# Kernel optimization log

Measured on AMD Instinct MI355X. Metric: run time of the kernel, lower is better.

Reference implementation:

```python
import math
import jax, jax.numpy as jnp
import numpy as np

N_NODES = 100000
N_EDGES = 1600000
IN_DIM, HID_DIM, OUT_DIM = 8, 64, 112


def _glorot(key, fan_in, fan_out):
    lim = math.sqrt(6.0 / (fan_in + fan_out))
    return jax.random.uniform(key, (fan_in, fan_out), jnp.float32, -lim, lim)


def _layer_params(key, in_d, out_d):
    ks = jax.random.split(key, 8)
    return dict(
        Wq=_glorot(ks[0], in_d, out_d), bq=jnp.zeros((out_d,), jnp.float32),
        Wk=_glorot(ks[1], in_d, out_d), bk=jnp.zeros((out_d,), jnp.float32),
        Wv=_glorot(ks[2], in_d, out_d), bv=jnp.zeros((out_d,), jnp.float32),
        Ws=_glorot(ks[3], in_d, out_d), bs=jnp.zeros((out_d,), jnp.float32),
    )


def setup_inputs() -> dict:
    key = jax.random.key(0)
    kx, ke, k0, k1, k2 = jax.random.split(key, 5)
    inp = {
        'x': jax.random.normal(kx, (N_NODES, IN_DIM), jnp.float32),
        'edge_index': jax.random.randint(ke, (2, N_EDGES), 0, N_NODES, jnp.int64),
    }
    for li, (kk, ind, outd) in enumerate([(k0, IN_DIM, HID_DIM), (k1, HID_DIM, HID_DIM), (k2, HID_DIM, OUT_DIM)]):
        p = _layer_params(kk, ind, outd)
        for name, v in p.items():
            inp[f'{name}{li}'] = v
    return inp


def _transformer_conv(x, src, dst, Wq, bq, Wk, bk, Wv, bv, Ws, bs):
    # heads=1, concat=True, no edge_attr, eval mode (no dropout)
    N = x.shape[0]
    C = Wq.shape[1]
    q = x @ Wq + bq            # [N, C]
    k = x @ Wk + bk
    v = x @ Wv + bv
    # per-edge attention score: <q_dst, k_src> / sqrt(C)
    scores = jnp.sum(q[dst] * k[src], axis=-1) * (1.0 / math.sqrt(C))  # [E]
    # segment softmax over destination neighborhoods (stable)
    m = jax.ops.segment_max(scores, dst, num_segments=N)               # [N]
    e = jnp.exp(scores - m[dst])                                       # [E]
    denom = jax.ops.segment_sum(e, dst, num_segments=N)                # [N]
    alpha = e / denom[dst]                                             # [E]
    # weighted scatter-add of source values to destinations
    out = jax.ops.segment_sum(alpha[:, None] * v[src], dst, num_segments=N)  # [N, C]
    # root/skip connection
    return out + (x @ Ws + bs)


def reference(x, edge_index,
              Wq0, bq0, Wk0, bk0, Wv0, bv0, Ws0, bs0,
              Wq1, bq1, Wk1, bk1, Wv1, bv1, Ws1, bs1,
              Wq2, bq2, Wk2, bk2, Wv2, bv2, Ws2, bs2):
    src, dst = edge_index[0], edge_index[1]
    h = _transformer_conv(x, src, dst, Wq0, bq0, Wk0, bk0, Wv0, bv0, Ws0, bs0)
    h = jax.nn.relu(h)
    h = _transformer_conv(h, src, dst, Wq1, bq1, Wk1, bk1, Wv1, bv1, Ws1, bs1)
    h = jax.nn.relu(h)
    out = _transformer_conv(h, src, dst, Wq2, bq2, Wk2, bk2, Wv2, bv2, Ws2, bs2)
    return out
```

## Files before the change

kernel.cpp:

```cpp
#include <hip/hip_runtime.h>
#include <hip/hip_fp16.h>
#include <math.h>
#include <float.h>
#include <stdint.h>

#define NN 100000
#define NE 1600000

#define SCAN_T 256
#define SCAN_E 1024
#define SCAN_NB ((NN + SCAN_E - 1) / SCAN_E)

#define NBUCK ((NN + 255) / 256)
#define EPB   4096
#define NBLK  ((NE + EPB - 1) / EPB)
#define HISTN (NBUCK * NBLK)
#define GS_NB ((HISTN + SCAN_E - 1) / SCAN_E)
#define BCAP  5120

typedef __attribute__((ext_vector_type(8))) short short8v;
typedef __attribute__((ext_vector_type(4))) float float4v;

__device__ __forceinline__ unsigned short f32_to_bf16_rne(float f) {
    unsigned u = __float_as_uint(f);
    u += 0x7FFFu + ((u >> 16) & 1u);
    return (unsigned short)(u >> 16);
}
__device__ __forceinline__ float bf16_to_f32(unsigned short h) {
    return __uint_as_float(((unsigned)h) << 16);
}

template<int K, int OUT>
__global__ __launch_bounds__(256)
void prep_w(const float* __restrict__ Wq, const float* __restrict__ Wk,
            const float* __restrict__ Wv, const float* __restrict__ Ws,
            unsigned short* __restrict__ wsp) {
    constexpr int NKS  = (K + 31) / 32;
    constexpr int OUTT = 4 * OUT;
    constexpr int NCT  = OUTT / 16;
    int idx = blockIdx.x * 256 + threadIdx.x;
    if (idx >= NCT * NKS * 512) return;
    int j    = idx & 7;
    int lane = (idx >> 3) & 63;
    int cell = idx >> 9;
    int ks   = cell % NKS;
    int ct   = cell / NKS;
    int g = lane >> 4, ln = lane & 15;
    int k = ks * 32 + g * 8 + j;
    int c = ct * 16 + ln;
    int mat = c / OUT, cm = c % OUT;
    const float* W = (mat == 0) ? Wq : (mat == 1) ? Wk : (mat == 2) ? Wv : Ws;
    float f = (k < K) ? W[(size_t)k * OUT + cm] : 0.f;
    unsigned short h = f32_to_bf16_rne(f);
    float resid = f - bf16_to_f32(h);
    wsp[(size_t)cell * 1024 + lane * 8 + j]       = h;
    wsp[(size_t)cell * 1024 + 512 + lane * 8 + j] = f32_to_bf16_rne(resid);
}

template<int K, int OUT, int CTSPLIT>
__global__ __launch_bounds__(256)
void gemm_qkvs(const float* __restrict__ x,
               const unsigned short* __restrict__ wsp,
               const float* __restrict__ bq, const float* __restrict__ bk,
               const float* __restrict__ bv, const float* __restrict__ bs,
               float* __restrict__ q, unsigned short* __restrict__ kv,
               float* __restrict__ outskip) {
    constexpr int NKS  = (K + 31) / 32;
    constexpr int OUTT = 4 * OUT;
    constexpr int NCT  = OUTT / 16;
    constexpr int CTPB = NCT / CTSPLIT;

    const int t    = threadIdx.x;
    const int lane = t & 63;
    const int wv   = t >> 6;
    const int g    = lane >> 4;
    const int ln   = lane & 15;
    const int rowbase = (blockIdx.x * 4 + wv) * 32;
    if (rowbase >= NN) return;

    union F8 { short8v v; unsigned short s[8]; uint4 u4; };

    F8 ahi[2][NKS], alo[2][NKS];
#pragma unroll
    for (int rt = 0; rt < 2; ++rt) {
        int r = rowbase + rt * 16 + ln;
        if (r >= NN) r = NN - 1;
        const float* rowp = x + (size_t)r * K;
#pragma unroll
        for (int ks = 0; ks < NKS; ++ks) {
            const int k0 = ks * 32 + g * 8;
            float xv[8];
            if (k0 + 8 <= K) {
                float4 p0 = *(const float4*)(rowp + k0);
                float4 p1 = *(const float4*)(rowp + k0 + 4);
                xv[0] = p0.x; xv[1] = p0.y; xv[2] = p0.z; xv[3] = p0.w;
                xv[4] = p1.x; xv[5] = p1.y; xv[6] = p1.z; xv[7] = p1.w;
            } else {
#pragma unroll
                for (int j = 0; j < 8; ++j) xv[j] = 0.f;
            }
#pragma unroll
            for (int j = 0; j < 8; ++j) {
                unsigned short h = f32_to_bf16_rne(xv[j]);
                ahi[rt][ks].s[j] = h;
                alo[rt][ks].s[j] = f32_to_bf16_rne(xv[j] - bf16_to_f32(h));
            }
        }
    }

    const int ct0 = blockIdx.y * CTPB;
#pragma unroll 1
    for (int ct = ct0; ct < ct0 + CTPB; ++ct) {
        F8 bhi[NKS], blo[NKS];
        const unsigned short* wp = wsp + (size_t)(ct * NKS) * 1024 + lane * 8;
#pragma unroll
        for (int ks = 0; ks < NKS; ++ks) {
            bhi[ks].u4 = *(const uint4*)(wp + ks * 1024);
            blo[ks].u4 = *(const uint4*)(wp + ks * 1024 + 512);
        }

        const int cb  = ct * 16;
        const int mat = cb / OUT;
        const int cm  = (cb % OUT) + ln;
        const float* B = (mat == 0) ? bq : (mat == 1) ? bk : (mat == 2) ? bv : bs;
        const float bias = B[cm];
        float4v acc0 = {bias, bias, bias, bias};
        float4v acc1 = {bias, bias, bias, bias};
#pragma unroll
        for (int ks = 0; ks < NKS; ++ks) {
            acc0 = __builtin_amdgcn_mfma_f32_16x16x32_bf16(ahi[0][ks].v, blo[ks].v, acc0, 0, 0, 0);
            acc0 = __builtin_amdgcn_mfma_f32_16x16x32_bf16(alo[0][ks].v, bhi[ks].v, acc0, 0, 0, 0);
            acc0 = __builtin_amdgcn_mfma_f32_16x16x32_bf16(ahi[0][ks].v, bhi[ks].v, acc0, 0, 0, 0);
            acc1 = __builtin_amdgcn_mfma_f32_16x16x32_bf16(ahi[1][ks].v, blo[ks].v, acc1, 0, 0, 0);
            acc1 = __builtin_amdgcn_mfma_f32_16x16x32_bf16(alo[1][ks].v, bhi[ks].v, acc1, 0, 0, 0);
            acc1 = __builtin_amdgcn_mfma_f32_16x16x32_bf16(ahi[1][ks].v, bhi[ks].v, acc1, 0, 0, 0);
        }

        if (mat == 0 || mat == 3) {
            float* dst = (mat == 0) ? q : outskip;
#pragma unroll
            for (int rt = 0; rt < 2; ++rt) {
                float4v a = rt ? acc1 : acc0;
#pragma unroll
                for (int reg = 0; reg < 4; ++reg) {
                    int node = rowbase + rt * 16 + g * 4 + reg;
                    if (node < NN)
                        dst[(size_t)node * OUT + cm] = a[reg];
                }
            }
        } else {
            const int base = (mat == 1) ? 0 : OUT;
#pragma unroll
            for (int rt = 0; rt < 2; ++rt) {
                float4v a = rt ? acc1 : acc0;
#pragma unroll
                for (int reg = 0; reg < 4; ++reg) {
                    int node = rowbase + rt * 16 + g * 4 + reg;
                    float f = a[reg];
                    float other = __shfl_xor(f, 1);
                    if (node < NN && !(ln & 1)) {
                        unsigned lo16 = __half_as_ushort(__float2half_rn(f));
                        unsigned hi16 = __half_as_ushort(__float2half_rn(other));
                        *(unsigned*)(kv + (size_t)node * (2 * OUT) + base + cm)
                            = lo16 | (hi16 << 16);
                    }
                }
            }
        }
    }
}

__global__ __launch_bounds__(256)
void bin_count(const int* __restrict__ ei, int* __restrict__ hist) {
    __shared__ int h[NBUCK];
    const int t = threadIdx.x;
    for (int i = t; i < NBUCK; i += 256) h[i] = 0;
    __syncthreads();
    int e0 = blockIdx.x * EPB;
    int e1 = e0 + EPB < NE ? e0 + EPB : NE;
    for (int i = e0 + t; i < e1; i += 256)
        atomicAdd(&h[ei[NE + i] >> 8], 1);
    __syncthreads();
    for (int i = t; i < NBUCK; i += 256)
        hist[(size_t)i * NBLK + blockIdx.x] = h[i];
}

__global__ __launch_bounds__(SCAN_T)
void gscan1(int* __restrict__ a, int* __restrict__ bsums) {
    __shared__ int lds[SCAN_T];
    int t = threadIdx.x;
    int base = blockIdx.x * SCAN_E + t * 4;
    int vals[4];
    int s = 0;
#pragma unroll
    for (int j = 0; j < 4; ++j) {
        int idx = base + j;
        vals[j] = (idx < HISTN) ? a[idx] : 0;
        s += vals[j];
    }
    lds[t] = s;
    __syncthreads();
    for (int off = 1; off < SCAN_T; off <<= 1) {
        int xx = (t >= off) ? lds[t - off] : 0;
        __syncthreads();
        lds[t] += xx;
        __syncthreads();
    }
    int run = (t > 0) ? lds[t - 1] : 0;
    if (t == SCAN_T - 1) bsums[blockIdx.x] = lds[t];
#pragma unroll
    for (int j = 0; j < 4; ++j) {
        int idx = base + j;
        if (idx < HISTN) a[idx] = run;
        run += vals[j];
    }
}

__global__ __launch_bounds__(256)
void gscan2(int* __restrict__ bsums) {
    __shared__ int lds[256];
    int t = threadIdx.x;
    lds[t] = (t < GS_NB) ? bsums[t] : 0;
    __syncthreads();
    for (int off = 1; off < 256; off <<= 1) {
        int xx = (t >= off) ? lds[t - off] : 0;
        __syncthreads();
        lds[t] += xx;
        __syncthreads();
    }
    if (t < GS_NB) bsums[t] = (t > 0) ? lds[t - 1] : 0;
}

__global__ __launch_bounds__(256)
void gscan3(int* __restrict__ a, const int* __restrict__ bsums,
            int* __restrict__ bstart) {
    int i = blockIdx.x * 256 + threadIdx.x;
    if (i < HISTN) {
        int v = a[i] + bsums[i / SCAN_E];
        a[i] = v;
        if (i % NBLK == 0) bstart[i / NBLK] = v;
    }
    if (i == 0) bstart[NBUCK] = NE;
}

__global__ __launch_bounds__(256)
void bin_scatter(const int* __restrict__ ei, const int* __restrict__ hist,
                 unsigned* __restrict__ ebuf) {
    __shared__ int off[NBUCK];
    const int t = threadIdx.x;
    for (int i = t; i < NBUCK; i += 256)
        off[i] = hist[(size_t)i * NBLK + blockIdx.x];
    __syncthreads();
    int e0 = blockIdx.x * EPB;
    int e1 = e0 + EPB < NE ? e0 + EPB : NE;
    for (int i = e0 + t; i < e1; i += 256) {
        int src = ei[i];
        int dst = ei[NE + i];
        int b = dst >> 8;
        int p = atomicAdd(&off[b], 1);
        ebuf[p] = ((unsigned)(dst & 255) << 17) | (unsigned)src;
    }
}

__global__ __launch_bounds__(256)
void bucket_hist(const int* __restrict__ bstart,
                 const unsigned* __restrict__ ebuf,
                 int* __restrict__ counts) {
    __shared__ int h[256];
    const int b = blockIdx.x;
    const int t = threadIdx.x;
    h[t] = 0;
    __syncthreads();
    int beg = bstart[b], end = bstart[b + 1];
    for (int i = beg + t; i < end; i += 256)
        atomicAdd(&h[ebuf[i] >> 17], 1);
    __syncthreads();
    int d = b * 256 + t;
    if (d < NN) counts[d] = h[t];
}

__global__ __launch_bounds__(SCAN_T)
void scan1(const int* __restrict__ counts, int* __restrict__ offsets,
           int* __restrict__ blocksums) {
    __shared__ int lds[SCAN_T];
    int t = threadIdx.x;
    int base = blockIdx.x * SCAN_E + t * 4;
    int vals[4];
    int s = 0;
#pragma unroll
    for (int j = 0; j < 4; ++j) {
        int idx = base + j;
        vals[j] = (idx < NN) ? counts[idx] : 0;
        s += vals[j];
    }
    lds[t] = s;
    __syncthreads();
    for (int off = 1; off < SCAN_T; off <<= 1) {
        int xx = (t >= off) ? lds[t - off] : 0;
        __syncthreads();
        lds[t] += xx;
        __syncthreads();
    }
    int run = (t > 0) ? lds[t - 1] : 0;
    if (t == SCAN_T - 1) blocksums[blockIdx.x] = lds[t];
#pragma unroll
    for (int j = 0; j < 4; ++j) {
        int idx = base + j;
        if (idx < NN) offsets[idx] = run;
        run += vals[j];
    }
}

__global__ __launch_bounds__(128)
void scan2(int* __restrict__ blocksums) {
    __shared__ int lds[128];
    int t = threadIdx.x;
    lds[t] = (t < SCAN_NB) ? blocksums[t] : 0;
    __syncthreads();
    for (int off = 1; off < 128; off <<= 1) {
        int xx = (t >= off) ? lds[t - off] : 0;
        __syncthreads();
        lds[t] += xx;
        __syncthreads();
    }
    if (t < SCAN_NB) blocksums[t] = (t > 0) ? lds[t - 1] : 0;
}

__global__ __launch_bounds__(256)
void scan3(int* __restrict__ offsets, const int* __restrict__ blocksums) {
    int i = blockIdx.x * blockDim.x + threadIdx.x;
    if (i < NN) offsets[i] = offsets[i] + blocksums[i / SCAN_E];
    if (i == 0) offsets[NN] = NE;
}

__global__ __launch_bounds__(256)
void csr_write(const int* __restrict__ bstart,
               const unsigned* __restrict__ ebuf,
               const int* __restrict__ offsets,
               int* __restrict__ sorted_src) {
    __shared__ int h[256];
    __shared__ int pre[256];
    __shared__ int posi[256];
    __shared__ unsigned srt[BCAP];
    const int b = blockIdx.x;
    const int t = threadIdx.x;
    h[t] = 0;
    __syncthreads();
    int beg = bstart[b];
    int cnt = bstart[b + 1] - beg;
    cnt = cnt < BCAP ? cnt : BCAP;
    const unsigned* buf = ebuf + beg;
    for (int i = t; i < cnt; i += 256)
        atomicAdd(&h[buf[i] >> 17], 1);
    __syncthreads();
    int v = h[t];
    pre[t] = v;
    __syncthreads();
    for (int off = 1; off < 256; off <<= 1) {
        int xx = (t >= off) ? pre[t - off] : 0;
        __syncthreads();
        pre[t] += xx;
        __syncthreads();
    }
    posi[t] = pre[t] - v;
    __syncthreads();
    for (int i = t; i < cnt; i += 256) {
        unsigned u = buf[i];
        int dl = u >> 17;
        int p = atomicAdd(&posi[dl], 1);
        srt[p] = u & 0x1FFFFu;
    }
    __syncthreads();
    const int base = offsets[b << 8];
    for (int i = t; i < cnt; i += 256)
        sorted_src[base + i] = (int)srt[i];
}

__device__ __forceinline__ float row16_sum(float x) {
    int y;
    y = __builtin_amdgcn_update_dpp(0, __float_as_int(x), 0x121, 0xF, 0xF, true); x += __int_as_float(y);
    y = __builtin_amdgcn_update_dpp(0, __float_as_int(x), 0x122, 0xF, 0xF, true); x += __int_as_float(y);
    y = __builtin_amdgcn_update_dpp(0, __float_as_int(x), 0x124, 0xF, 0xF, true); x += __int_as_float(y);
    y = __builtin_amdgcn_update_dpp(0, __float_as_int(x), 0x128, 0xF, 0xF, true); x += __int_as_float(y);
    return x;
}

__device__ __forceinline__ float4 h4_to_f4(uint2 w) {
    union { unsigned u; __half2 h; } a, b;
    a.u = w.x; b.u = w.y;
    float2 f0 = __half22float2(a.h);
    float2 f1 = __half22float2(b.h);
    return make_float4(f0.x, f0.y, f1.x, f1.y);
}

template<int C, bool RELU>
__global__ __launch_bounds__(256)
void attn_gather(const int* __restrict__ offsets,
                 const int* __restrict__ sorted_src,
                 const float* __restrict__ q,
                 const unsigned short* __restrict__ kv,
                 float* __restrict__ out, float scale) {
    const int wid  = (int)((blockIdx.x * blockDim.x + threadIdx.x) >> 6);
    const int lane = threadIdx.x & 63;
    if (wid >= NN) return;
    const int grp = lane >> 4;
    const int ch  = (lane & 15) * 4;
    constexpr bool P2 = (C > 64);
    const bool hi = P2 && (ch + 64 < C);

    const int beg = offsets[wid], end = offsets[wid + 1];

    float4 qv0 = *(const float4*)(q + (size_t)wid * C + ch);
    float4 qv1 = make_float4(0.f, 0.f, 0.f, 0.f);
    if (hi) qv1 = *(const float4*)(q + (size_t)wid * C + ch + 64);

    float m = -FLT_MAX, l = 0.f;
    float4 a0 = make_float4(0.f, 0.f, 0.f, 0.f);
    float4 a1 = make_float4(0.f, 0.f, 0.f, 0.f);

    int i = beg + grp;
    uint2 kw0 = make_uint2(0, 0), vw0 = kw0, kw1 = kw0, vw1 = kw0;
    if (i < end) {
        const unsigned short* row = kv + (size_t)sorted_src[i] * (2 * C);
        kw0 = *(const uint2*)(row + ch);
        vw0 = *(const uint2*)(row + C + ch);
        if (hi) {
            kw1 = *(const uint2*)(row + 64 + ch);
            vw1 = *(const uint2*)(row + C + 64 + ch);
        }
    }
    while (i < end) {
        int inext = i + 4;
        uint2 nkw0 = make_uint2(0, 0), nvw0 = nkw0, nkw1 = nkw0, nvw1 = nkw0;
        if (inext < end) {
            const unsigned short* row = kv + (size_t)sorted_src[inext] * (2 * C);
            nkw0 = *(const uint2*)(row + ch);
            nvw0 = *(const uint2*)(row + C + ch);
            if (hi) {
                nkw1 = *(const uint2*)(row + 64 + ch);
                nvw1 = *(const uint2*)(row + C + 64 + ch);
            }
        }
        float4 kf0 = h4_to_f4(kw0);
        float4 vf0 = h4_to_f4(vw0);
        float part = qv0.x * kf0.x + qv0.y * kf0.y + qv0.z * kf0.z + qv0.w * kf0.w;
        float4 kf1, vf1;
        if (P2) {
            kf1 = h4_to_f4(kw1);
            vf1 = h4_to_f4(vw1);
            part += qv1.x * kf1.x + qv1.y * kf1.y + qv1.z * kf1.z + qv1.w * kf1.w;
        }
        float s = row16_sum(part) * scale;
        float mn = fmaxf(m, s);
        float al = __expf(m - mn);
        float w  = __expf(s - mn);
        l = l * al + w;
        a0.x = a0.x * al + w * vf0.x; a0.y = a0.y * al + w * vf0.y;
        a0.z = a0.z * al + w * vf0.z; a0.w = a0.w * al + w * vf0.w;
        if (P2) {
            a1.x = a1.x * al + w * vf1.x; a1.y = a1.y * al + w * vf1.y;
            a1.z = a1.z * al + w * vf1.z; a1.w = a1.w * al + w * vf1.w;
        }
        m = mn;
        kw0 = nkw0; vw0 = nvw0; kw1 = nkw1; vw1 = nvw1;
        i = inext;
    }

#pragma unroll
    for (int d = 16; d <= 32; d <<= 1) {
        float mo = __shfl_xor(m, d);
        float lo = __shfl_xor(l, d);
        float4 ao0, ao1;
        ao0.x = __shfl_xor(a0.x, d); ao0.y = __shfl_xor(a0.y, d);
        ao0.z = __shfl_xor(a0.z, d); ao0.w = __shfl_xor(a0.w, d);
        if (P2) {
            ao1.x = __shfl_xor(a1.x, d); ao1.y = __shfl_xor(a1.y, d);
            ao1.z = __shfl_xor(a1.z, d); ao1.w = __shfl_xor(a1.w, d);
        }
        float mn = fmaxf(m, mo);
        float e1 = (l  > 0.f) ? __expf(m  - mn) : 0.f;
        float e2 = (lo > 0.f) ? __expf(mo - mn) : 0.f;
        l = l * e1 + lo * e2;
        a0.x = a0.x * e1 + ao0.x * e2; a0.y = a0.y * e1 + ao0.y * e2;
        a0.z = a0.z * e1 + ao0.z * e2; a0.w = a0.w * e1 + ao0.w * e2;
        if (P2) {
            a1.x = a1.x * e1 + ao1.x * e2; a1.y = a1.y * e1 + ao1.y * e2;
            a1.z = a1.z * e1 + ao1.z * e2; a1.w = a1.w * e1 + ao1.w * e2;
        }
        m = mn;
    }

    if (lane < 16) {
        float inv = (l > 0.f) ? 1.f / l : 0.f;
        size_t o = (size_t)wid * C + ch;
        float4 sk = *(const float4*)(out + o);
        float4 r;
        r.x = sk.x + a0.x * inv; r.y = sk.y + a0.y * inv;
        r.z = sk.z + a0.z * inv; r.w = sk.w + a0.w * inv;
        if (RELU) {
            r.x = fmaxf(r.x, 0.f); r.y = fmaxf(r.y, 0.f);
            r.z = fmaxf(r.z, 0.f); r.w = fmaxf(r.w, 0.f);
        }
        *(float4*)(out + o) = r;
        if (hi) {
            float4 sk1 = *(const float4*)(out + o + 64);
            float4 r1;
            r1.x = sk1.x + a1.x * inv; r1.y = sk1.y + a1.y * inv;
            r1.z = sk1.z + a1.z * inv; r1.w = sk1.w + a1.w * inv;
            if (RELU) {
                r1.x = fmaxf(r1.x, 0.f); r1.y = fmaxf(r1.y, 0.f);
                r1.z = fmaxf(r1.z, 0.f); r1.w = fmaxf(r1.w, 0.f);
            }
            *(float4*)(out + o + 64) = r1;
        }
    }
}

template<int K, int OUT, bool RELU>
static void run_layer(const float* xin, const unsigned short* wsp,
                      const float* const* Wb,
                      const int* offsets, const int* sorted_src,
                      float* q, unsigned short* kv,
                      float* out, hipStream_t stream) {
    constexpr int CTSPLIT = 2;
    dim3 gg((NN + 127) / 128, CTSPLIT);
    gemm_qkvs<K, OUT, CTSPLIT><<<gg, 256, 0, stream>>>(
        xin, wsp, Wb[1], Wb[3], Wb[5], Wb[7], q, kv, out);

    float scale = 1.0f / sqrtf((float)OUT);
    attn_gather<OUT, RELU><<<(NN + 3) / 4, 256, 0, stream>>>(
        offsets, sorted_src, q, kv, out, scale);
}

extern "C" void kernel_launch(void* const* d_in, const int* in_sizes, int n_in,
                              void* d_out, int out_size, void* d_ws, size_t ws_size,
                              hipStream_t stream) {
    const float* x  = (const float*)d_in[0];
    const int*   ei = (const int*)d_in[1];
    const float* Wb0[8], *Wb1[8], *Wb2[8];
    for (int i = 0; i < 8; ++i) {
        Wb0[i] = (const float*)d_in[2 + i];
        Wb1[i] = (const float*)d_in[10 + i];
        Wb2[i] = (const float*)d_in[18 + i];
    }
    float* out = (float*)d_out;

    char* ws = (char*)d_ws;
    const size_t CMAX = 112;
    size_t off = 0;
    float*          q  = (float*)(ws + off);          off += (size_t)NN * CMAX * 4;
    unsigned short* kv = (unsigned short*)(ws + off); off += (size_t)NN * 2 * CMAX * 2;
    float* h0          = (float*)(ws + off);          off += (size_t)NN * 64 * 4;
    float* h1          = (float*)(ws + off);          off += (size_t)NN * 64 * 4;
    int*   sorted_src  = (int*)(ws + off);            off += (size_t)NE * 4;
    int*   counts      = (int*)(ws + off);            off += (size_t)NN * 4;
    int*   offsets     = (int*)(ws + off);            off += (size_t)(NN + 1) * 4;
    int*   blocksums   = (int*)(ws + off);            off += (size_t)SCAN_NB * 4;
    int*   hist        = (int*)(ws + off);            off += (size_t)HISTN * 4;
    int*   gsums       = (int*)(ws + off);            off += (size_t)GS_NB * 4;
    int*   bstart      = (int*)(ws + off);            off += (size_t)(NBUCK + 1) * 4;
    unsigned* ebuf     = (unsigned*)(ws + off);       off += (size_t)NE * 4;
    (void)ws_size; (void)in_sizes; (void)n_in; (void)out_size;

    bin_count<<<NBLK, 256, 0, stream>>>(ei, hist);
    gscan1<<<GS_NB, SCAN_T, 0, stream>>>(hist, gsums);
    gscan2<<<1, 256, 0, stream>>>(gsums);
    gscan3<<<(HISTN + 255) / 256, 256, 0, stream>>>(hist, gsums, bstart);
    bin_scatter<<<NBLK, 256, 0, stream>>>(ei, hist, ebuf);
    bucket_hist<<<NBUCK, 256, 0, stream>>>(bstart, ebuf, counts);
    scan1<<<SCAN_NB, SCAN_T, 0, stream>>>(counts, offsets, blocksums);
    scan2<<<1, 128, 0, stream>>>(blocksums);
    scan3<<<(NN + 255) / 256, 256, 0, stream>>>(offsets, blocksums);
    csr_write<<<NBUCK, 256, 0, stream>>>(bstart, ebuf, offsets, sorted_src);

    unsigned short* wspbase =
        (unsigned short*)(((uintptr_t)ebuf + 255) & ~(uintptr_t)255);
    unsigned short* wsp0 = wspbase;
    unsigned short* wsp1 = wsp0 + 16 * 1 * 1024;
    unsigned short* wsp2 = wsp1 + 16 * 2 * 1024;
    prep_w<8, 64><<<(16 * 1 * 512 + 255) / 256, 256, 0, stream>>>(
        Wb0[0], Wb0[2], Wb0[4], Wb0[6], wsp0);
    prep_w<64, 64><<<(16 * 2 * 512 + 255) / 256, 256, 0, stream>>>(
        Wb1[0], Wb1[2], Wb1[4], Wb1[6], wsp1);
    prep_w<64, 112><<<(28 * 2 * 512 + 255) / 256, 256, 0, stream>>>(
        Wb2[0], Wb2[2], Wb2[4], Wb2[6], wsp2);

    run_layer<8,  64, true >(x,  wsp0, Wb0, offsets, sorted_src, q, kv, h0,  stream);
    run_layer<64, 64, true >(h0, wsp1, Wb1, offsets, sorted_src, q, kv, h1,  stream);
    run_layer<64, 112, false>(h1, wsp2, Wb2, offsets, sorted_src, q, kv, out, stream);
}
```

Before: 555.7 us.

## Interleave K/V rows per channel group, prefetch two edges ahead, use exp2

The projection kernel now stores K and V interleaved in groups of four channels, so each lane fetches its K and V slice with one 16-byte load instead of two 8-byte loads. The gather loop prefetches two edges ahead instead of one to hide more random-access latency. The attention scale and log2(e) are folded into q once, and the exponentials use the hardware exp2 instruction, removing a multiply per edge. The deeper prefetch raises register use and may lower occupancy.

```diff
diff --git a/kernel.cpp b/kernel.cpp
--- a/kernel.cpp
+++ b/kernel.cpp
@@ -149,7 +149,8 @@
                 }
             }
         } else {
-            const int base = (mat == 1) ? 0 : OUT;
+            const int base = (mat == 1) ? 0 : 4;
+            const int kvoff = ((cm >> 2) * 8) + (cm & 3) + base;
 #pragma unroll
             for (int rt = 0; rt < 2; ++rt) {
                 float4v a = rt ? acc1 : acc0;
@@ -161,7 +162,7 @@
                     if (node < NN && !(ln & 1)) {
                         unsigned lo16 = __half_as_ushort(__float2half_rn(f));
                         unsigned hi16 = __half_as_ushort(__float2half_rn(other));
-                        *(unsigned*)(kv + (size_t)node * (2 * OUT) + base + cm)
+                        *(unsigned*)(kv + (size_t)node * (2 * OUT) + kvoff)
                             = lo16 | (hi16 << 16);
                     }
                 }
@@ -385,9 +386,9 @@
     return x;
 }
 
-__device__ __forceinline__ float4 h4_to_f4(uint2 w) {
+__device__ __forceinline__ float4 h4_to_f4(unsigned wx, unsigned wy) {
     union { unsigned u; __half2 h; } a, b;
-    a.u = w.x; b.u = w.y;
+    a.u = wx; b.u = wy;
     float2 f0 = __half22float2(a.h);
     float2 f1 = __half22float2(b.h);
     return make_float4(f0.x, f0.y, f1.x, f1.y);
@@ -410,50 +411,55 @@
 
     const int beg = offsets[wid], end = offsets[wid + 1];
 
+    const float sl = scale * 1.44269504f;
     float4 qv0 = *(const float4*)(q + (size_t)wid * C + ch);
+    qv0.x *= sl; qv0.y *= sl; qv0.z *= sl; qv0.w *= sl;
     float4 qv1 = make_float4(0.f, 0.f, 0.f, 0.f);
-    if (hi) qv1 = *(const float4*)(q + (size_t)wid * C + ch + 64);
+    if (hi) {
+        qv1 = *(const float4*)(q + (size_t)wid * C + ch + 64);
+        qv1.x *= sl; qv1.y *= sl; qv1.z *= sl; qv1.w *= sl;
+    }
 
     float m = -FLT_MAX, l = 0.f;
     float4 a0 = make_float4(0.f, 0.f, 0.f, 0.f);
     float4 a1 = make_float4(0.f, 0.f, 0.f, 0.f);
 
+    const uint4 zz = make_uint4(0, 0, 0, 0);
+    uint4 A0 = zz, A1 = zz, B0 = zz, B1 = zz;
+
     int i = beg + grp;
-    uint2 kw0 = make_uint2(0, 0), vw0 = kw0, kw1 = kw0, vw1 = kw0;
     if (i < end) {
         const unsigned short* row = kv + (size_t)sorted_src[i] * (2 * C);
-        kw0 = *(const uint2*)(row + ch);
-        vw0 = *(const uint2*)(row + C + ch);
-        if (hi) {
-            kw1 = *(const uint2*)(row + 64 + ch);
-            vw1 = *(const uint2*)(row + C + 64 + ch);
-        }
-    }
+        A0 = *(const uint4*)(row + 2 * ch);
+        if (hi) A1 = *(const uint4*)(row + 2 * ch + 128);
+    }
+    if (i + 4 < end) {
+        const unsigned short* row = kv + (size_t)sorted_src[i + 4] * (2 * C);
+        B0 = *(const uint4*)(row + 2 * ch);
+        if (hi) B1 = *(const uint4*)(row + 2 * ch + 128);
+    }
+
     while (i < end) {
-        int inext = i + 4;
-        uint2 nkw0 = make_uint2(0, 0), nvw0 = nkw0, nkw1 = nkw0, nvw1 = nkw0;
-        if (inext < end) {
-            const unsigned short* row = kv + (size_t)sorted_src[inext] * (2 * C);
-            nkw0 = *(const uint2*)(row + ch);
-            nvw0 = *(const uint2*)(row + C + ch);
-            if (hi) {
-                nkw1 = *(const uint2*)(row + 64 + ch);
-                nvw1 = *(const uint2*)(row + C + 64 + ch);
-            }
-        }
-        float4 kf0 = h4_to_f4(kw0);
-        float4 vf0 = h4_to_f4(vw0);
+        uint4 N0 = zz, N1 = zz;
+        int ip = i + 8;
+        if (ip < end) {
+            const unsigned short* row = kv + (size_t)sorted_src[ip] * (2 * C);
+            N0 = *(const uint4*)(row + 2 * ch);
+            if (hi) N1 = *(const uint4*)(row + 2 * ch + 128);
+        }
+        float4 kf0 = h4_to_f4(A0.x, A0.y);
+        float4 vf0 = h4_to_f4(A0.z, A0.w);
         float part = qv0.x * kf0.x + qv0.y * kf0.y + qv0.z * kf0.z + qv0.w * kf0.w;
-        float4 kf1, vf1;
+        float4 vf1 = make_float4(0.f, 0.f, 0.f, 0.f);
         if (P2) {
-            kf1 = h4_to_f4(kw1);
-            vf1 = h4_to_f4(vw1);
+            float4 kf1 = h4_to_f4(A1.x, A1.y);
+            vf1 = h4_to_f4(A1.z, A1.w);
             part += qv1.x * kf1.x + qv1.y * kf1.y + qv1.z * kf1.z + qv1.w * kf1.w;
         }
-        float s = row16_sum(part) * scale;
+        float s = row16_sum(part);
         float mn = fmaxf(m, s);
-        float al = __expf(m - mn);
-        float w  = __expf(s - mn);
+        float al = __builtin_amdgcn_exp2f(m - mn);
+        float w  = __builtin_amdgcn_exp2f(s - mn);
         l = l * al + w;
         a0.x = a0.x * al + w * vf0.x; a0.y = a0.y * al + w * vf0.y;
         a0.z = a0.z * al + w * vf0.z; a0.w = a0.w * al + w * vf0.w;
@@ -462,8 +468,8 @@
             a1.z = a1.z * al + w * vf1.z; a1.w = a1.w * al + w * vf1.w;
         }
         m = mn;
-        kw0 = nkw0; vw0 = nvw0; kw1 = nkw1; vw1 = nvw1;
-        i = inext;
+        A0 = B0; A1 = B1; B0 = N0; B1 = N1;
+        i += 4;
     }
 
 #pragma unroll
@@ -478,8 +484,8 @@
             ao1.z = __shfl_xor(a1.z, d); ao1.w = __shfl_xor(a1.w, d);
         }
         float mn = fmaxf(m, mo);
-        float e1 = (l  > 0.f) ? __expf(m  - mn) : 0.f;
-        float e2 = (lo > 0.f) ? __expf(mo - mn) : 0.f;
+        float e1 = (l  > 0.f) ? __builtin_amdgcn_exp2f(m  - mn) : 0.f;
+        float e2 = (lo > 0.f) ? __builtin_amdgcn_exp2f(mo - mn) : 0.f;
         l = l * e1 + lo * e2;
         a0.x = a0.x * e1 + ao0.x * e2; a0.y = a0.y * e1 + ao0.y * e2;
         a0.z = a0.z * e1 + ao0.z * e2; a0.w = a0.w * e1 + ao0.w * e2;
```

Measured after the change: 551.7 us. No clear change (-0.7%).
